# Kernel tuning notes

Measured on AMD Instinct MI355X. Metric: run time of the kernel, lower is better.

Reference implementation:

```python
import jax, jax.numpy as jnp
import numpy as np

N, E = 50000, 800000
F_IN, H, P, C = 128, 64, 16, 40
L = 3  # gcn_layers


def setup_inputs() -> dict:
    key = jax.random.key(0)
    ks = jax.random.split(key, 10)
    s = 0.05
    return {
        "x_h": jax.random.normal(ks[0], (N, F_IN), jnp.float32),
        "pos_feat": jax.random.normal(ks[1], (N, P), jnp.float32),
        "edge_index": jax.random.randint(ks[2], (2, E), 0, N, dtype=jnp.int32),
        "W_pos": jax.random.normal(ks[3], (P, H), jnp.float32) * s,
        "b_pos": jnp.zeros((H,), jnp.float32),
        "W_init": jax.random.normal(ks[4], (F_IN, H), jnp.float32) * s,
        "b_init": jnp.zeros((H,), jnp.float32),
        "W_l": jax.random.normal(ks[5], (L, H, H), jnp.float32) * s,  # neighbor weight
        "W_r": jax.random.normal(ks[6], (L, H, H), jnp.float32) * s,  # root weight
        "b_conv": jnp.zeros((L, H), jnp.float32),
        "W_last": jax.random.normal(ks[7], (H, C), jnp.float32) * s,
        "b_last": jnp.zeros((C,), jnp.float32),
    }


def _sage_conv(x, src, dst, Wl, Wr, b):
    # PyG SAGEConv(aggr='mean'): out_i = Wl @ mean_{j in N(i)} x_j + Wr @ x_i + b
    msgs = x[src]  # [E, H] gather of source-node features
    agg = jax.ops.segment_sum(msgs, dst, num_segments=N)
    cnt = jax.ops.segment_sum(jnp.ones((E,), x.dtype), dst, num_segments=N)
    agg = agg / jnp.clip(cnt, 1.0, None)[:, None]  # mean; deg-0 nodes -> 0
    return agg @ Wl + x @ Wr + b


def reference(x_h, pos_feat, edge_index, W_pos, b_pos, W_init, b_init,
              W_l, W_r, b_conv, W_last, b_last):
    src, dst = edge_index[0], edge_index[1]
    # pos_embedding -> (hyperbolic encode simplified to identity in Euclidean manifold) -> tanh
    hyp_pos = jnp.tanh(pos_feat @ W_pos + b_pos)  # [N, H]
    h = x_h @ W_init + b_init  # [N, H]
    for i in range(L):
        h = _sage_conv(h, src, dst, W_l[i], W_r[i], b_conv[i])
        if i != L - 1:
            h = h + hyp_pos       # run_base == 'False' branch
            h = jax.nn.relu(h)    # dropout is no-op in eval mode
    emb = h @ W_last + b_last     # [N, C]
    return emb, jax.nn.log_softmax(emb, axis=1)
```

## Files before the change

kernel.cpp:

```cpp
#include <hip/hip_runtime.h>
#include <hip/hip_bf16.h>

#define NN 50000
#define NE 800000
#define FIN 128
#define HD 64
#define NC 40
#define XG   782
#define NB   391
#define NBK  782
#define BW   64

typedef __hip_bfloat16 bf16;
typedef __attribute__((ext_vector_type(8))) short bf16x8;
typedef __attribute__((ext_vector_type(4))) float f32x4;

__device__ __forceinline__ void acc8(float* a, uint4 v){
  a[0] += __uint_as_float(v.x << 16); a[1] += __uint_as_float(v.x & 0xffff0000u);
  a[2] += __uint_as_float(v.y << 16); a[3] += __uint_as_float(v.y & 0xffff0000u);
  a[4] += __uint_as_float(v.z << 16); a[5] += __uint_as_float(v.z & 0xffff0000u);
  a[6] += __uint_as_float(v.w << 16); a[7] += __uint_as_float(v.w & 0xffff0000u);
}

__device__ __forceinline__ unsigned pack2(float lo, float hi){
  union { bf16 b; unsigned short u; } a, b;
  a.b = __float2bfloat16(lo);
  b.b = __float2bfloat16(hi);
  return (unsigned)a.u | ((unsigned)b.u << 16);
}

__device__ __forceinline__ short f2bf_bits(float f){
  union { bf16 b; short s; } u;
  u.b = __float2bfloat16(f);
  return u.s;
}

__device__ __forceinline__ void init_body(
    int wid, const float* __restrict__ x, const float* __restrict__ pos,
    const float* __restrict__ Wi, const float* __restrict__ bi,
    const float* __restrict__ Wp, const float* __restrict__ bp,
    bf16* __restrict__ h0b, bf16* __restrict__ hypb, int lane){
  const int quad = lane >> 4;
  const int col  = lane & 15;
  const int nw   = XG * 4;

  bf16x8 wif[4][4];
  #pragma unroll
  for (int ct = 0; ct < 4; ++ct)
    #pragma unroll
    for (int kf = 0; kf < 4; ++kf)
      #pragma unroll
      for (int j = 0; j < 8; ++j)
        wif[ct][kf][j] = f2bf_bits(Wi[(kf*32 + quad*8 + j)*HD + ct*16 + col]);
  bf16x8 wpf[4];
  #pragma unroll
  for (int ct = 0; ct < 4; ++ct)
    #pragma unroll
    for (int j = 0; j < 8; ++j){
      const int k = quad*8 + j;
      wpf[ct][j] = (k < 16) ? f2bf_bits(Wp[k*HD + ct*16 + col]) : (short)0;
    }
  float bih[4], bph[4];
  #pragma unroll
  for (int c = 0; c < 4; ++c){ bih[c] = bi[c*16 + col]; bph[c] = bp[c*16 + col]; }

  for (int t = wid; t < NN/16; t += nw){
    const int n0 = t * 16;
    bf16x8 af[4];
    #pragma unroll
    for (int kf = 0; kf < 4; ++kf){
      const float* xr = x + (size_t)(n0 + col)*FIN + kf*32 + quad*8;
      const float4 f0 = *(const float4*)xr;
      const float4 f1 = *(const float4*)(xr + 4);
      af[kf][0] = f2bf_bits(f0.x); af[kf][1] = f2bf_bits(f0.y);
      af[kf][2] = f2bf_bits(f0.z); af[kf][3] = f2bf_bits(f0.w);
      af[kf][4] = f2bf_bits(f1.x); af[kf][5] = f2bf_bits(f1.y);
      af[kf][6] = f2bf_bits(f1.z); af[kf][7] = f2bf_bits(f1.w);
    }
    bf16x8 ap;
    #pragma unroll
    for (int j = 0; j < 8; ++j) ap[j] = 0;
    if (quad < 2){
      const float* pr = pos + (size_t)(n0 + col)*16 + quad*8;
      const float4 p0 = *(const float4*)pr;
      const float4 p1 = *(const float4*)(pr + 4);
      ap[0] = f2bf_bits(p0.x); ap[1] = f2bf_bits(p0.y);
      ap[2] = f2bf_bits(p0.z); ap[3] = f2bf_bits(p0.w);
      ap[4] = f2bf_bits(p1.x); ap[5] = f2bf_bits(p1.y);
      ap[6] = f2bf_bits(p1.z); ap[7] = f2bf_bits(p1.w);
    }
    f32x4 ah[4], app[4];
    #pragma unroll
    for (int c = 0; c < 4; ++c){
      ah[c]  = (f32x4){bih[c], bih[c], bih[c], bih[c]};
      app[c] = (f32x4){bph[c], bph[c], bph[c], bph[c]};
    }
    #pragma unroll
    for (int ct = 0; ct < 4; ++ct){
      #pragma unroll
      for (int kf = 0; kf < 4; ++kf)
        ah[ct] = __builtin_amdgcn_mfma_f32_16x16x32_bf16(af[kf], wif[ct][kf], ah[ct], 0, 0, 0);
      app[ct] = __builtin_amdgcn_mfma_f32_16x16x32_bf16(ap, wpf[ct], app[ct], 0, 0, 0);
    }
    #pragma unroll
    for (int reg = 0; reg < 4; ++reg){
      const int n = n0 + quad*4 + reg;
      #pragma unroll
      for (int c = 0; c < 4; ++c){
        h0b[(size_t)n*HD + c*16 + col]  = __float2bfloat16(ah[c][reg]);
        hypb[(size_t)n*HD + c*16 + col] = __float2bfloat16(tanhf(app[c][reg]));
      }
    }
  }
}

__global__ __launch_bounds__(256) void k_hist(
    const int* __restrict__ ei, int* __restrict__ hist, int* __restrict__ totals,
    const float* __restrict__ x, const float* __restrict__ pos,
    const float* __restrict__ Wi, const float* __restrict__ bi,
    const float* __restrict__ Wp, const float* __restrict__ bp,
    bf16* __restrict__ h0b, bf16* __restrict__ hypb){
  __shared__ int lh[NBK];
  if (blockIdx.x < NB){
    for (int i = threadIdx.x; i < NBK; i += 256) lh[i] = 0;
    __syncthreads();
    int e = blockIdx.x * 2048 + threadIdx.x;
    #pragma unroll
    for (int j = 0; j < 8; ++j, e += 256)
      if (e < NE) atomicAdd(&lh[ei[NE + e] >> 6], 1);
    __syncthreads();
    for (int i = threadIdx.x; i < NBK; i += 256){
      const int c = lh[i];
      hist[i*NB + blockIdx.x] = c;
      if (c) atomicAdd(&totals[i], c);
    }
    return;
  }
  init_body((blockIdx.x - NB) * 4 + (threadIdx.x >> 6),
            x, pos, Wi, bi, Wp, bp, h0b, hypb, threadIdx.x & 63);
}

__global__ __launch_bounds__(512) void k_scan(
    const int* __restrict__ hist, const int* __restrict__ totals,
    int* __restrict__ ofs, int* __restrict__ baseA){
  __shared__ int sc[512];
  __shared__ int baseSh;
  const int b = blockIdx.x;
  const int t = threadIdx.x;
  int part = 0;
  for (int j = t; j < b; j += 512) part += totals[j];
  sc[t] = part; __syncthreads();
  for (int off = 256; off > 0; off >>= 1){
    if (t < off) sc[t] += sc[t + off];
    __syncthreads();
  }
  if (t == 0) baseSh = sc[0];
  __syncthreads();
  const int base = baseSh;
  __syncthreads();
  const int v = (t < NB) ? hist[b*NB + t] : 0;
  sc[t] = v; __syncthreads();
  for (int off = 1; off < 512; off <<= 1){
    const int xv = (t >= off) ? sc[t - off] : 0;
    __syncthreads();
    sc[t] += xv;
    __syncthreads();
  }
  if (t < NB) ofs[b*NB + t] = base + sc[t] - v;
  if (t == 0) baseA[b] = base;
  if (b == NBK - 1 && t == 0) baseA[NBK] = base + sc[511];
}

__global__ __launch_bounds__(256) void k_scatter(
    const int* __restrict__ ei, const int* __restrict__ ofs,
    int* __restrict__ packed){
  __shared__ int cur[NBK];
  for (int i = threadIdx.x; i < NBK; i += 256) cur[i] = ofs[i*NB + blockIdx.x];
  __syncthreads();
  int e = blockIdx.x * 2048 + threadIdx.x;
  #pragma unroll
  for (int j = 0; j < 8; ++j, e += 256){
    if (e < NE){
      const int d = ei[NE + e];
      const int s = ei[e];
      const int p = atomicAdd(&cur[d >> 6], 1);
      packed[p] = s | ((d & 63) << 16);
    }
  }
}

__global__ __launch_bounds__(256) void k_ell(
    const int* __restrict__ packed, const int* __restrict__ baseA,
    int* __restrict__ esrc, int* __restrict__ degp){
  __shared__ int cnt[BW];
  __shared__ int ell[BW * 64];
  if (threadIdx.x < BW) cnt[threadIdx.x] = 0;
  __syncthreads();
  const int b  = blockIdx.x;
  const int lo = baseA[b], hi = baseA[b + 1];
  for (int e = lo + threadIdx.x; e < hi; e += 256){
    const int pk = packed[e];
    const int dl = (pk >> 16) & 63;
    const int p  = atomicAdd(&cnt[dl], 1);
    if (p < 64) ell[dl*64 + p] = pk & 0xffff;
  }
  __syncthreads();
  const int n0 = b * BW;
  for (int i = threadIdx.x; i < BW * 16; i += 256){
    const int node = i >> 4;
    if (n0 + node < NN)
      ((uint4*)(esrc + (size_t)(n0 + node)*64))[i & 15] = ((const uint4*)ell)[i];
  }
  for (int i = threadIdx.x; i < BW; i += 256)
    if (n0 + i < NN) degp[n0 + i] = cnt[i];
}

__global__ __launch_bounds__(256) void k_xform(
    const bf16* __restrict__ h, const float* __restrict__ Wl,
    const float* __restrict__ Wr, const float* __restrict__ bc,
    const bf16* __restrict__ hypb, const int use_hyp,
    bf16* __restrict__ y, bf16* __restrict__ z){
  const int lane = threadIdx.x & 63;
  const int quad = lane >> 4;
  const int col  = lane & 15;
  const int wid  = blockIdx.x * 4 + (threadIdx.x >> 6);
  const int nw   = gridDim.x * 4;

  bf16x8 bfr[8][2];
  #pragma unroll
  for (int ct = 0; ct < 8; ++ct){
    const float* W = (ct < 4) ? Wl : Wr;
    const int nc = (ct & 3) * 16 + col;
    #pragma unroll
    for (int kf = 0; kf < 2; ++kf)
      #pragma unroll
      for (int j = 0; j < 8; ++j)
        bfr[ct][kf][j] = f2bf_bits(W[(kf*32 + quad*8 + j)*HD + nc]);
  }
  float zb[4];
  #pragma unroll
  for (int c = 0; c < 4; ++c) zb[c] = bc[c*16 + col];

  for (int t = wid; t < NN/16; t += nw){
    const int n0 = t * 16;
    union { uint4 u; bf16x8 v; } a0, a1;
    a0.u = *(const uint4*)(h + (size_t)(n0 + col)*HD + quad*8);
    a1.u = *(const uint4*)(h + (size_t)(n0 + col)*HD + 32 + quad*8);
    f32x4 acc[8];
    #pragma unroll
    for (int c = 0; c < 4; ++c) acc[c] = (f32x4){0.f, 0.f, 0.f, 0.f};
    #pragma unroll
    for (int c = 0; c < 4; ++c) acc[4+c] = (f32x4){zb[c], zb[c], zb[c], zb[c]};
    #pragma unroll
    for (int ct = 0; ct < 8; ++ct){
      acc[ct] = __builtin_amdgcn_mfma_f32_16x16x32_bf16(a0.v, bfr[ct][0], acc[ct], 0, 0, 0);
      acc[ct] = __builtin_amdgcn_mfma_f32_16x16x32_bf16(a1.v, bfr[ct][1], acc[ct], 0, 0, 0);
    }
    #pragma unroll
    for (int reg = 0; reg < 4; ++reg){
      const int n = n0 + quad*4 + reg;
      #pragma unroll
      for (int c = 0; c < 4; ++c){
        y[(size_t)n*HD + c*16 + col] = __float2bfloat16(acc[c][reg]);
        float zv = acc[4+c][reg];
        if (use_hyp) zv += __bfloat162float(hypb[(size_t)n*HD + c*16 + col]);
        z[(size_t)n*HD + c*16 + col] = __float2bfloat16(zv);
      }
    }
  }
}

__global__ __launch_bounds__(256) void k_gather(
    const bf16* __restrict__ y, const bf16* __restrict__ z,
    const int* __restrict__ degp, const int* __restrict__ esrc,
    bf16* __restrict__ out, const int do_relu){
  const int lane  = threadIdx.x & 63;
  const int n     = blockIdx.x * 4 + (threadIdx.x >> 6);
  if (n >= NN) return;
  const int fq    = lane & 7;
  const int eslot = lane >> 3;
  const int deg   = min(degp[n], 64);
  const int r0    = n << 6;
  const int r1    = r0 + deg;
  float a0[8] = {0,0,0,0,0,0,0,0};
  float a1[8] = {0,0,0,0,0,0,0,0};
  int e = r0 + eslot;
  for (; e + 8 < r1; e += 16){
    const int s0 = esrc[e];
    const int s1 = esrc[e + 8];
    const uint4 v0 = ((const uint4*)(y + (size_t)s0*HD))[fq];
    const uint4 v1 = ((const uint4*)(y + (size_t)s1*HD))[fq];
    acc8(a0, v0);
    acc8(a1, v1);
  }
  if (e < r1){
    const int s = esrc[e];
    const uint4 v = ((const uint4*)(y + (size_t)s*HD))[fq];
    acc8(a0, v);
  }
  #pragma unroll
  for (int j = 0; j < 8; ++j){
    float s = a0[j] + a1[j];
    s += __shfl_xor(s, 8, 64);
    s += __shfl_xor(s, 16, 64);
    s += __shfl_xor(s, 32, 64);
    a0[j] = s;
  }
  if (eslot == 0){
    const float inv = deg > 0 ? 1.f / (float)deg : 0.f;
    const uint4 zv = ((const uint4*)(z + (size_t)n*HD))[fq];
    float zf[8];
    zf[0] = __uint_as_float(zv.x << 16); zf[1] = __uint_as_float(zv.x & 0xffff0000u);
    zf[2] = __uint_as_float(zv.y << 16); zf[3] = __uint_as_float(zv.y & 0xffff0000u);
    zf[4] = __uint_as_float(zv.z << 16); zf[5] = __uint_as_float(zv.z & 0xffff0000u);
    zf[6] = __uint_as_float(zv.w << 16); zf[7] = __uint_as_float(zv.w & 0xffff0000u);
    float o[8];
    #pragma unroll
    for (int j = 0; j < 8; ++j){
      o[j] = a0[j]*inv + zf[j];
      if (do_relu) o[j] = fmaxf(o[j], 0.f);
    }
    uint4 pv;
    pv.x = pack2(o[0], o[1]);
    pv.y = pack2(o[2], o[3]);
    pv.z = pack2(o[4], o[5]);
    pv.w = pack2(o[6], o[7]);
    ((uint4*)(out + (size_t)n*HD))[fq] = pv;
  }
}

__global__ __launch_bounds__(256) void k_final(
    const bf16* __restrict__ hin, const float* __restrict__ Wl,
    const float* __restrict__ bl, float* __restrict__ out){
  const int lane = threadIdx.x & 63;
  const int quad = lane >> 4;
  const int col  = lane & 15;
  const int wid  = blockIdx.x * 4 + (threadIdx.x >> 6);
  const int nw   = gridDim.x * 4;

  bf16x8 wf[3][2];
  float bb[3];
  #pragma unroll
  for (int ct = 0; ct < 3; ++ct){
    const int nc = ct*16 + col;
    const bool valid = nc < NC;
    bb[ct] = valid ? bl[nc] : -1e30f;
    #pragma unroll
    for (int kf = 0; kf < 2; ++kf)
      #pragma unroll
      for (int j = 0; j < 8; ++j)
        wf[ct][kf][j] = valid ? f2bf_bits(Wl[(kf*32 + quad*8 + j)*NC + nc]) : (short)0;
  }

  for (int t = wid; t < NN/16; t += nw){
    const int n0 = t * 16;
    union { uint4 u; bf16x8 v; } a0, a1;
    a0.u = *(const uint4*)(hin + (size_t)(n0 + col)*HD + quad*8);
    a1.u = *(const uint4*)(hin + (size_t)(n0 + col)*HD + 32 + quad*8);
    f32x4 acc[3];
    #pragma unroll
    for (int ct = 0; ct < 3; ++ct){
      acc[ct] = (f32x4){bb[ct], bb[ct], bb[ct], bb[ct]};
      acc[ct] = __builtin_amdgcn_mfma_f32_16x16x32_bf16(a0.v, wf[ct][0], acc[ct], 0, 0, 0);
      acc[ct] = __builtin_amdgcn_mfma_f32_16x16x32_bf16(a1.v, wf[ct][1], acc[ct], 0, 0, 0);
    }
    #pragma unroll
    for (int reg = 0; reg < 4; ++reg){
      const float e0 = acc[0][reg], e1 = acc[1][reg], e2 = acc[2][reg];
      float vmax = fmaxf(fmaxf(e0, e1), e2);
      vmax = fmaxf(vmax, __shfl_xor(vmax, 1, 64));
      vmax = fmaxf(vmax, __shfl_xor(vmax, 2, 64));
      vmax = fmaxf(vmax, __shfl_xor(vmax, 4, 64));
      vmax = fmaxf(vmax, __shfl_xor(vmax, 8, 64));
      float s = __expf(e0 - vmax) + __expf(e1 - vmax) + __expf(e2 - vmax);
      s += __shfl_xor(s, 1, 64);
      s += __shfl_xor(s, 2, 64);
      s += __shfl_xor(s, 4, 64);
      s += __shfl_xor(s, 8, 64);
      const float off = vmax + __logf(s);
      const int n = n0 + quad*4 + reg;
      #pragma unroll
      for (int ct = 0; ct < 3; ++ct){
        const int nc = ct*16 + col;
        if (nc < NC){
          const float e = acc[ct][reg];
          out[(size_t)n*NC + nc]                 = e;
          out[(size_t)NN*NC + (size_t)n*NC + nc] = e - off;
        }
      }
    }
  }
}

extern "C" void kernel_launch(void* const* d_in, const int* in_sizes, int n_in,
                              void* d_out, int out_size, void* d_ws, size_t ws_size,
                              hipStream_t stream){
  (void)in_sizes; (void)n_in; (void)out_size; (void)ws_size;
  const float* x_h    = (const float*)d_in[0];
  const float* pos    = (const float*)d_in[1];
  const int*   ei     = (const int*)  d_in[2];
  const float* W_pos  = (const float*)d_in[3];
  const float* b_pos  = (const float*)d_in[4];
  const float* W_init = (const float*)d_in[5];
  const float* b_init = (const float*)d_in[6];
  const float* W_l    = (const float*)d_in[7];
  const float* W_r    = (const float*)d_in[8];
  const float* b_conv = (const float*)d_in[9];
  const float* W_last = (const float*)d_in[10];
  const float* b_last = (const float*)d_in[11];
  float* out = (float*)d_out;

  char* p = (char*)d_ws;
  auto alloc = [&](size_t bytes)->char*{
    char* r = p; p += (bytes + 255) & ~(size_t)255; return r;
  };
  bf16* hb0  = (bf16*)alloc((size_t)NN*HD*2);
  bf16* hb1  = (bf16*)alloc((size_t)NN*HD*2);
  bf16* yb   = (bf16*)alloc((size_t)NN*HD*2);
  bf16* zbuf = (bf16*)alloc((size_t)NN*HD*2);
  bf16* hypb = (bf16*)alloc((size_t)NN*HD*2);
  int* esrc  = (int*)alloc((size_t)NN*64*4);
  int* degp  = (int*)alloc((size_t)NN*4);

  int* hist   = (int*)yb;
  int* ofs    = hist + NBK*NB;
  int* totals = ofs + NBK*NB;
  int* baseA  = totals + NBK;
  int* packed = (int*)zbuf;

  hipMemsetAsync(totals, 0, (size_t)NBK*4, stream);
  k_hist   <<<NB + XG, 256, 0, stream>>>(ei, hist, totals, x_h, pos,
                                         W_init, b_init, W_pos, b_pos, hb0, hypb);
  k_scan   <<<NBK, 512, 0, stream>>>(hist, totals, ofs, baseA);
  k_scatter<<<NB, 256, 0, stream>>>(ei, ofs, packed);
  k_ell    <<<NBK, 256, 0, stream>>>(packed, baseA, esrc, degp);

  bf16* cur = hb0;
  bf16* nxt = hb1;
  for (int l = 0; l < 3; ++l){
    const int last = (l == 2);
    k_xform <<<XG, 256, 0, stream>>>(cur, W_l + l*HD*HD, W_r + l*HD*HD,
                                     b_conv + l*HD, hypb, !last, yb, zbuf);
    k_gather<<<(NN + 3)/4, 256, 0, stream>>>(yb, zbuf, degp, esrc, nxt, !last);
    bf16* t = cur; cur = nxt; nxt = t;
  }
  k_final <<<XG, 256, 0, stream>>>(cur, W_last, b_last, out);
}
```

Before: 275.8 us.

## Split scan into per-bucket and global passes, store ELL sources as 16-bit

The histogram is now stored transposed with no global atomics for totals, so the memset goes away. The old single scan kernel had every block re-sum all earlier bucket totals. It is replaced by a per-bucket scan plus a single-block scan over bucket totals, and the scatter kernel adds the two offsets. The ELL source-index table is shrunk from 32-bit to 16-bit entries, which halves the index traffic in the gather kernels. The 16-bit entries depend on source ids fitting in 16 bits, and N=50000 is below 65536. The transposed histogram read in scanA is strided and uncoalesced.

Measured after the change: 261.6 us. 1.05x faster.

```diff
diff --git a/kernel.cpp b/kernel.cpp
--- a/kernel.cpp
+++ b/kernel.cpp
@@ -115,7 +115,7 @@
 }
 
 __global__ __launch_bounds__(256) void k_hist(
-    const int* __restrict__ ei, int* __restrict__ hist, int* __restrict__ totals,
+    const int* __restrict__ ei, int* __restrict__ histT,
     const float* __restrict__ x, const float* __restrict__ pos,
     const float* __restrict__ Wi, const float* __restrict__ bi,
     const float* __restrict__ Wp, const float* __restrict__ bp,
@@ -129,36 +129,21 @@
     for (int j = 0; j < 8; ++j, e += 256)
       if (e < NE) atomicAdd(&lh[ei[NE + e] >> 6], 1);
     __syncthreads();
-    for (int i = threadIdx.x; i < NBK; i += 256){
-      const int c = lh[i];
-      hist[i*NB + blockIdx.x] = c;
-      if (c) atomicAdd(&totals[i], c);
-    }
+    for (int i = threadIdx.x; i < NBK; i += 256)
+      histT[blockIdx.x*NBK + i] = lh[i];
     return;
   }
   init_body((blockIdx.x - NB) * 4 + (threadIdx.x >> 6),
             x, pos, Wi, bi, Wp, bp, h0b, hypb, threadIdx.x & 63);
 }
 
-__global__ __launch_bounds__(512) void k_scan(
-    const int* __restrict__ hist, const int* __restrict__ totals,
-    int* __restrict__ ofs, int* __restrict__ baseA){
+__global__ __launch_bounds__(512) void k_scanA(
+    const int* __restrict__ histT, int* __restrict__ ofsT,
+    int* __restrict__ totals){
   __shared__ int sc[512];
-  __shared__ int baseSh;
   const int b = blockIdx.x;
   const int t = threadIdx.x;
-  int part = 0;
-  for (int j = t; j < b; j += 512) part += totals[j];
-  sc[t] = part; __syncthreads();
-  for (int off = 256; off > 0; off >>= 1){
-    if (t < off) sc[t] += sc[t + off];
-    __syncthreads();
-  }
-  if (t == 0) baseSh = sc[0];
-  __syncthreads();
-  const int base = baseSh;
-  __syncthreads();
-  const int v = (t < NB) ? hist[b*NB + t] : 0;
+  const int v = (t < NB) ? histT[t*NBK + b] : 0;
   sc[t] = v; __syncthreads();
   for (int off = 1; off < 512; off <<= 1){
     const int xv = (t >= off) ? sc[t - off] : 0;
@@ -166,16 +151,32 @@
     sc[t] += xv;
     __syncthreads();
   }
-  if (t < NB) ofs[b*NB + t] = base + sc[t] - v;
-  if (t == 0) baseA[b] = base;
-  if (b == NBK - 1 && t == 0) baseA[NBK] = base + sc[511];
+  if (t < NB) ofsT[t*NBK + b] = sc[t] - v;
+  if (t == 511) totals[b] = sc[511];
+}
+
+__global__ __launch_bounds__(1024) void k_scanB(
+    const int* __restrict__ totals, int* __restrict__ baseA){
+  __shared__ int sc[1024];
+  const int t = threadIdx.x;
+  const int v = (t < NBK) ? totals[t] : 0;
+  sc[t] = v; __syncthreads();
+  for (int off = 1; off < 1024; off <<= 1){
+    const int xv = (t >= off) ? sc[t - off] : 0;
+    __syncthreads();
+    sc[t] += xv;
+    __syncthreads();
+  }
+  if (t < NBK) baseA[t] = sc[t] - v;
+  if (t == 1023) baseA[NBK] = sc[1023];
 }
 
 __global__ __launch_bounds__(256) void k_scatter(
-    const int* __restrict__ ei, const int* __restrict__ ofs,
-    int* __restrict__ packed){
+    const int* __restrict__ ei, const int* __restrict__ ofsT,
+    const int* __restrict__ baseA, int* __restrict__ packed){
   __shared__ int cur[NBK];
-  for (int i = threadIdx.x; i < NBK; i += 256) cur[i] = ofs[i*NB + blockIdx.x];
+  for (int i = threadIdx.x; i < NBK; i += 256)
+    cur[i] = baseA[i] + ofsT[blockIdx.x*NBK + i];
   __syncthreads();
   int e = blockIdx.x * 2048 + threadIdx.x;
   #pragma unroll
@@ -191,9 +192,9 @@
 
 __global__ __launch_bounds__(256) void k_ell(
     const int* __restrict__ packed, const int* __restrict__ baseA,
-    int* __restrict__ esrc, int* __restrict__ degp){
+    unsigned short* __restrict__ esrc, int* __restrict__ degp){
   __shared__ int cnt[BW];
-  __shared__ int ell[BW * 64];
+  __shared__ unsigned short ell[BW * 64];
   if (threadIdx.x < BW) cnt[threadIdx.x] = 0;
   __syncthreads();
   const int b  = blockIdx.x;
@@ -202,14 +203,14 @@
     const int pk = packed[e];
     const int dl = (pk >> 16) & 63;
     const int p  = atomicAdd(&cnt[dl], 1);
-    if (p < 64) ell[dl*64 + p] = pk & 0xffff;
+    if (p < 64) ell[dl*64 + p] = (unsigned short)(pk & 0xffff);
   }
   __syncthreads();
   const int n0 = b * BW;
-  for (int i = threadIdx.x; i < BW * 16; i += 256){
-    const int node = i >> 4;
+  for (int i = threadIdx.x; i < BW * 8; i += 256){
+    const int node = i >> 3;
     if (n0 + node < NN)
-      ((uint4*)(esrc + (size_t)(n0 + node)*64))[i & 15] = ((const uint4*)ell)[i];
+      ((uint4*)(esrc + (size_t)(n0 + node)*64))[i & 7] = ((const uint4*)ell)[i];
   }
   for (int i = threadIdx.x; i < BW; i += 256)
     if (n0 + i < NN) degp[n0 + i] = cnt[i];
@@ -272,7 +273,7 @@
 
 __global__ __launch_bounds__(256) void k_gather(
     const bf16* __restrict__ y, const bf16* __restrict__ z,
-    const int* __restrict__ degp, const int* __restrict__ esrc,
+    const int* __restrict__ degp, const unsigned short* __restrict__ esrc,
     bf16* __restrict__ out, const int do_relu){
   const int lane  = threadIdx.x & 63;
   const int n     = blockIdx.x * 4 + (threadIdx.x >> 6);
@@ -419,20 +420,20 @@
   bf16* yb   = (bf16*)alloc((size_t)NN*HD*2);
   bf16* zbuf = (bf16*)alloc((size_t)NN*HD*2);
   bf16* hypb = (bf16*)alloc((size_t)NN*HD*2);
-  int* esrc  = (int*)alloc((size_t)NN*64*4);
+  unsigned short* esrc = (unsigned short*)alloc((size_t)NN*64*2);
   int* degp  = (int*)alloc((size_t)NN*4);
 
-  int* hist   = (int*)yb;
-  int* ofs    = hist + NBK*NB;
-  int* totals = ofs + NBK*NB;
+  int* histT  = (int*)yb;
+  int* ofsT   = histT + NB*NBK;
+  int* totals = ofsT + NB*NBK;
   int* baseA  = totals + NBK;
   int* packed = (int*)zbuf;
 
-  hipMemsetAsync(totals, 0, (size_t)NBK*4, stream);
-  k_hist   <<<NB + XG, 256, 0, stream>>>(ei, hist, totals, x_h, pos,
+  k_hist   <<<NB + XG, 256, 0, stream>>>(ei, histT, x_h, pos,
                                          W_init, b_init, W_pos, b_pos, hb0, hypb);
-  k_scan   <<<NBK, 512, 0, stream>>>(hist, totals, ofs, baseA);
-  k_scatter<<<NB, 256, 0, stream>>>(ei, ofs, packed);
+  k_scanA  <<<NBK, 512, 0, stream>>>(histT, ofsT, totals);
+  k_scanB  <<<1, 1024, 0, stream>>>(totals, baseA);
+  k_scatter<<<NB, 256, 0, stream>>>(ei, ofsT, baseA, packed);
   k_ell    <<<NBK, 256, 0, stream>>>(packed, baseA, esrc, degp);
 
   bf16* cur = hb0;
```
